# Optimization experiments

Measured on AMD Instinct MI355X. Metric: run time of the kernel, lower is better.

## Reference

```python
import jax, jax.numpy as jnp
import numpy as np

EPS = 1e-5

def _layernorm(x, g, b):
    mu = jnp.mean(x, axis=-1, keepdims=True)
    var = jnp.mean(jnp.square(x - mu), axis=-1, keepdims=True)
    return (x - mu) * jax.lax.rsqrt(var + EPS) * g + b

def _time_shift(x):
    # xx[:, t] = x[:, t-1], xx[:, 0] = 0  (ZeroPad2d((0,0,1,-1)))
    return jnp.pad(x, ((0, 0), (1, 0), (0, 0)))[:, :-1, :]

def _wkv(time_decay, time_first, k, v):
    # Numerically-stable RWKV v4 recurrence (matches wkv_cuda forward).
    # k, v: [B, T, C]; time_decay, time_first: [C]
    w = -jnp.exp(time_decay)  # negative decay
    u = time_first
    B, T, C = k.shape
    aa0 = jnp.zeros((B, C), k.dtype)
    bb0 = jnp.zeros((B, C), k.dtype)
    pp0 = jnp.full((B, C), -1e38, k.dtype)

    def step(carry, kv_t):
        aa, bb, pp = carry
        kt, vt = kv_t
        ww = u + kt
        p = jnp.maximum(pp, ww)
        e1 = jnp.exp(pp - p)
        e2 = jnp.exp(ww - p)
        yt = (e1 * aa + e2 * vt) / (e1 * bb + e2)
        ww2 = pp + w
        p2 = jnp.maximum(ww2, kt)
        e1b = jnp.exp(ww2 - p2)
        e2b = jnp.exp(kt - p2)
        return (e1b * aa + e2b * vt, e1b * bb + e2b, p2), yt

    kT = jnp.swapaxes(k, 0, 1)  # [T, B, C]
    vT = jnp.swapaxes(v, 0, 1)
    _, y = jax.lax.scan(step, (aa0, bb0, pp0), (kT, vT))
    return jnp.swapaxes(y, 0, 1)  # [B, T, C]


def setup_inputs() -> dict:
    num_layers, layer_id, C = 8, 1, 512
    B, T = 512, 50
    H = 4 * C
    key = jax.random.key(0)
    ks = jax.random.split(key, 12)

    # parameter init mirroring the torch module's structured init
    ratio_0_to_1 = layer_id / (num_layers - 1)
    ratio_1_to_almost0 = 1.0 - layer_id / num_layers
    h = np.arange(C, dtype=np.float32)
    time_decay = (-5 + 8 * (h / (C - 1)) ** (0.7 + 1.3 * ratio_0_to_1)).astype(np.float32)
    zigzag = (np.array([(i + 1) % 3 - 1 for i in range(C)], dtype=np.float32)) * 0.5
    time_first = (np.ones(C, dtype=np.float32) * np.log(0.3) + zigzag).astype(np.float32)
    xr = (h / C).astype(np.float32)
    att_mix_k = (xr ** ratio_1_to_almost0)[None, None, :].astype(np.float32)
    att_mix_v = (xr ** ratio_1_to_almost0 + 0.3 * ratio_0_to_1)[None, None, :].astype(np.float32)
    att_mix_r = (xr ** (0.5 * ratio_1_to_almost0))[None, None, :].astype(np.float32)
    ffn_mix_k = att_mix_k.copy()
    ffn_mix_r = att_mix_k.copy()

    s = 0.02
    return {
        "x": jax.random.normal(ks[0], (B, T, C), jnp.float32),
        "ln1_g": jnp.ones((C,), jnp.float32), "ln1_b": jnp.zeros((C,), jnp.float32),
        "ln2_g": jnp.ones((C,), jnp.float32), "ln2_b": jnp.zeros((C,), jnp.float32),
        "att_mix_k": jnp.asarray(att_mix_k), "att_mix_v": jnp.asarray(att_mix_v),
        "att_mix_r": jnp.asarray(att_mix_r),
        "time_decay": jnp.asarray(time_decay), "time_first": jnp.asarray(time_first),
        "Wk": jax.random.normal(ks[1], (C, C), jnp.float32) * s,
        "Wv": jax.random.normal(ks[2], (C, C), jnp.float32) * s,
        "Wr": jax.random.normal(ks[3], (C, C), jnp.float32) * s,
        "Wo": jax.random.normal(ks[4], (C, C), jnp.float32) * s,
        "ffn_mix_k": jnp.asarray(ffn_mix_k), "ffn_mix_r": jnp.asarray(ffn_mix_r),
        "Fk": jax.random.normal(ks[5], (H, C), jnp.float32) * s,
        "Fv": jax.random.normal(ks[6], (C, H), jnp.float32) * s,
        "Fr": jax.random.normal(ks[7], (C, C), jnp.float32) * s,
    }


def reference(x, ln1_g, ln1_b, ln2_g, ln2_b,
              att_mix_k, att_mix_v, att_mix_r, time_decay, time_first,
              Wk, Wv, Wr, Wo, ffn_mix_k, ffn_mix_r, Fk, Fv, Fr):
    # --- time-mix (attention) branch ---
    h = _layernorm(x, ln1_g, ln1_b)
    hh = _time_shift(h)
    xk = h * att_mix_k + hh * (1 - att_mix_k)
    xv = h * att_mix_v + hh * (1 - att_mix_v)
    xr = h * att_mix_r + hh * (1 - att_mix_r)
    k = jnp.einsum('btc,dc->btd', xk, Wk)
    v = jnp.einsum('btc,dc->btd', xv, Wv)
    sr = jax.nn.sigmoid(jnp.einsum('btc,dc->btd', xr, Wr))
    rwkv = sr * _wkv(time_decay, time_first, k, v)
    x = x + jnp.einsum('btc,dc->btd', rwkv, Wo)

    # --- channel-mix (FFN) branch ---
    h = _layernorm(x, ln2_g, ln2_b)
    hh = _time_shift(h)
    fk = h * ffn_mix_k + hh * (1 - ffn_mix_k)
    fr = h * ffn_mix_r + hh * (1 - ffn_mix_r)
    kk = jnp.einsum('btc,hc->bth', fk, Fk)
    kk = jnp.square(jax.nn.relu(kk))
    kv = jnp.einsum('bth,ch->btc', kk, Fv)
    rkv = jax.nn.sigmoid(jnp.einsum('btc,dc->btd', fr, Fr)) * kv
    return x + rkv
```

## Files before the change

kernel.cpp:

```cpp
#include <hip/hip_runtime.h>
#include <stdint.h>

typedef unsigned short u16;
typedef __bf16 bf16x8 __attribute__((ext_vector_type(8)));
typedef float f32x4 __attribute__((ext_vector_type(4)));

#define DEV static __device__ __forceinline__

DEV u16 f2b(float f) {
    unsigned u = __float_as_uint(f);
    u += 0x7FFF + ((u >> 16) & 1);
    return (u16)(u >> 16);
}
DEV float b2f(u16 h) { return __uint_as_float((unsigned)h << 16); }

DEV void load16(const void* g, void* l) {
    __builtin_amdgcn_global_load_lds((const __attribute__((address_space(1))) void*)g,
                                     (__attribute__((address_space(3))) void*)l, 16, 0, 0);
}

__global__ __launch_bounds__(256) void cvt_all(
    const float* __restrict__ Wk, const float* __restrict__ Wv,
    const float* __restrict__ Wr, const float* __restrict__ Wo,
    const float* __restrict__ Fk, const float* __restrict__ Fv,
    const float* __restrict__ Fr, u16* __restrict__ dst) {
    const int CC = 512 * 512, HC = 2048 * 512;
    int e = (blockIdx.x * 256 + threadIdx.x) * 4;
    const float* s; int base;
    if      (e < 1 * CC)      { s = Wk; base = 0; }
    else if (e < 2 * CC)      { s = Wv; base = 1 * CC; }
    else if (e < 3 * CC)      { s = Wr; base = 2 * CC; }
    else if (e < 4 * CC)      { s = Wo; base = 3 * CC; }
    else if (e < 4 * CC + HC) { s = Fk; base = 4 * CC; }
    else if (e < 4 * CC + 2 * HC) { s = Fv; base = 4 * CC + HC; }
    else                      { s = Fr; base = 4 * CC + 2 * HC; }
    float4 f = *(const float4*)(s + (e - base));
    ushort4 o;
    o.x = f2b(f.x); o.y = f2b(f.y); o.z = f2b(f.z); o.w = f2b(f.w);
    *(ushort4*)(dst + e) = o;
}

template <int NOUT>
__global__ __launch_bounds__(256) void ln_seq(
    const float* __restrict__ x, const float* __restrict__ g, const float* __restrict__ be,
    const float* __restrict__ mk, const float* __restrict__ mv, const float* __restrict__ mr,
    u16* __restrict__ ok, u16* __restrict__ ov, u16* __restrict__ orr, int T) {
    const int C = 512;
    int b = blockIdx.x;
    int tid = threadIdx.x;
    int c = tid * 2;
    const float* xb = x + (size_t)b * T * C;
    float g0 = g[c], g1 = g[c + 1], be0 = be[c], be1 = be[c + 1];
    float k0 = mk[c], k1 = mk[c + 1];
    float v0 = 0.f, v1 = 0.f;
    if (NOUT == 3) { v0 = mv[c]; v1 = mv[c + 1]; }
    float r0 = mr[c], r1 = mr[c + 1];
    __shared__ float sm[2][8];
    float h0p = 0.f, h1p = 0.f;
    size_t idx = (size_t)b * T * C + c;
    for (int t = 0; t < T; ++t) {
        float2 vt = *(const float2*)(xb + (size_t)t * C + c);
        float s0 = vt.x + vt.y, s1 = vt.x * vt.x + vt.y * vt.y;
#pragma unroll
        for (int off = 32; off; off >>= 1) {
            s0 += __shfl_down(s0, off); s1 += __shfl_down(s1, off);
        }
        int w = tid >> 6;
        if ((tid & 63) == 0) { sm[t & 1][w * 2] = s0; sm[t & 1][w * 2 + 1] = s1; }
        __syncthreads();
        s0 = sm[t & 1][0] + sm[t & 1][2] + sm[t & 1][4] + sm[t & 1][6];
        s1 = sm[t & 1][1] + sm[t & 1][3] + sm[t & 1][5] + sm[t & 1][7];
        float mu = s0 * (1.f / 512.f);
        float var = s1 * (1.f / 512.f) - mu * mu;
        float rs = rsqrtf(var + 1e-5f);
        float h0 = (vt.x - mu) * rs * g0 + be0;
        float h1 = (vt.y - mu) * rs * g1 + be1;
        *(ushort2*)&ok[idx] = make_ushort2(f2b(h0 * k0 + h0p * (1.f - k0)),
                                           f2b(h1 * k1 + h1p * (1.f - k1)));
        if (NOUT == 3)
            *(ushort2*)&ov[idx] = make_ushort2(f2b(h0 * v0 + h0p * (1.f - v0)),
                                               f2b(h1 * v1 + h1p * (1.f - v1)));
        *(ushort2*)&orr[idx] = make_ushort2(f2b(h0 * r0 + h0p * (1.f - r0)),
                                            f2b(h1 * r1 + h1p * (1.f - r1)));
        h0p = h0; h1p = h1;
        idx += C;
    }
}

template <int EPI>
__global__ __launch_bounds__(256) void gemm128(
    const u16* __restrict__ A0, int strideAz,
    const u16* __restrict__ B0, int strideBz,
    void* O0, void* O1, void* O2,
    const float* __restrict__ Add, const u16* __restrict__ Mul,
    int K, int D) {
    const int BM = 128, BN = 128, BK = 64;
    __shared__ __align__(16) u16 As[2][BM * BK];
    __shared__ __align__(16) u16 Bs[2][BN * BK];

    int gx = gridDim.x, gy = gridDim.y;
    int fid = blockIdx.x + gx * (blockIdx.y + gy * blockIdx.z);
    int nwg = gx * gy * gridDim.z;
    int q = nwg >> 3, r = nwg & 7, xcd = fid & 7, jj = fid >> 3;
    int swz = (xcd < r ? xcd * (q + 1) : r * (q + 1) + (xcd - r) * q) + jj;
    int bx = swz % gx;
    int tmp = swz / gx;
    int by = tmp % gy;
    int bz = tmp / gy;

    const u16* A = A0 + (size_t)bz * strideAz;
    const u16* B = B0 + (size_t)bz * strideBz;
    void* Out = (bz == 0) ? O0 : (bz == 1) ? O1 : O2;

    int tid = threadIdx.x, lane = tid & 63, w = tid >> 6;
    int wm = w >> 1, wn = w & 1;
    int rowBase = by * BM, colBase = bx * BN;
    int l8 = lane >> 3;
    int gsrc = ((lane & 7) ^ l8) * 8;

    const int nt = K / BK;
    f32x4 acc[4][4] = {};

    auto stage = [&](int buf, int kt) {
#pragma unroll
        for (int i = 0; i < 4; ++i) {
            int rr0 = w * 32 + i * 8;
            load16(A + (size_t)(rowBase + rr0 + l8) * K + kt + gsrc, &As[buf][rr0 * BK]);
            load16(B + (size_t)(colBase + rr0 + l8) * K + kt + gsrc, &Bs[buf][rr0 * BK]);
        }
    };

    stage(0, 0);
    __syncthreads();
    int cur = 0;
    for (int t = 0; t < nt; ++t) {
        if (t + 1 < nt) stage(cur ^ 1, (t + 1) * BK);
#pragma unroll
        for (int s = 0; s < 2; ++s) {
            bf16x8 af[4], bfv[4];
#pragma unroll
            for (int m = 0; m < 4; ++m) {
                int row = wm * 64 + m * 16 + (lane & 15);
                int gsw = (s * 4 + (lane >> 4)) ^ (row & 7);
                af[m] = *(const bf16x8*)&As[cur][row * BK + gsw * 8];
            }
#pragma unroll
            for (int n = 0; n < 4; ++n) {
                int col = wn * 64 + n * 16 + (lane & 15);
                int gsw = (s * 4 + (lane >> 4)) ^ (col & 7);
                bfv[n] = *(const bf16x8*)&Bs[cur][col * BK + gsw * 8];
            }
#pragma unroll
            for (int m = 0; m < 4; ++m)
#pragma unroll
                for (int n = 0; n < 4; ++n)
                    acc[m][n] = __builtin_amdgcn_mfma_f32_16x16x32_bf16(af[m], bfv[n], acc[m][n], 0, 0, 0);
        }
        __syncthreads();
        cur ^= 1;
    }

    int r0e = (lane >> 4) * 4;
    int ce = lane & 15;
#pragma unroll
    for (int m = 0; m < 4; ++m) {
#pragma unroll
        for (int n = 0; n < 4; ++n) {
            int row = rowBase + wm * 64 + m * 16 + r0e;
            int col = colBase + wn * 64 + n * 16 + ce;
#pragma unroll
            for (int rr = 0; rr < 4; ++rr) {
                size_t idx = (size_t)(row + rr) * D + col;
                float v = acc[m][n][rr];
                if (EPI == 0) {
                    ((u16*)Out)[idx] = f2b(v);
                } else if (EPI == 2) {
                    ((float*)Out)[idx] = v + Add[idx];
                } else if (EPI == 3) {
                    float rl = fmaxf(v, 0.f);
                    ((u16*)Out)[idx] = f2b(rl * rl);
                } else if (EPI == 4) {
                    float s = 1.f / (1.f + __expf(-v));
                    ((float*)Out)[idx] = Add[idx] + s * b2f(Mul[idx]);
                } else {
                    ((u16*)Out)[idx] = (bz == 2) ? f2b(1.f / (1.f + __expf(-v))) : f2b(v);
                }
            }
        }
    }
}

__global__ __launch_bounds__(256) void wkv_kernel(
    const u16* __restrict__ k, const u16* __restrict__ v, const u16* __restrict__ sr,
    const float* __restrict__ td, const float* __restrict__ tf,
    u16* __restrict__ rwkv, int T) {
    const int C = 512;
    int gid = blockIdx.x * 256 + threadIdx.x;
    int c = gid & (C - 1);
    int b = gid >> 9;
    float w = -__expf(td[c]);
    float u = tf[c];
    float aa = 0.f, bb = 0.f, pp = -1e38f;
    size_t idx = (size_t)b * T * C + c;
    for (int t = 0; t < T; ++t, idx += C) {
        float kt = b2f(k[idx]), vt = b2f(v[idx]);
        float ww = u + kt;
        float p = fmaxf(pp, ww);
        float e1 = __expf(pp - p), e2 = __expf(ww - p);
        float y = (e1 * aa + e2 * vt) / (e1 * bb + e2);
        float ww2 = pp + w;
        float p2 = fmaxf(ww2, kt);
        float e1b = __expf(ww2 - p2), e2b = __expf(kt - p2);
        aa = e1b * aa + e2b * vt;
        bb = e1b * bb + e2b;
        pp = p2;
        rwkv[idx] = f2b(b2f(sr[idx]) * y);
    }
}

extern "C" void kernel_launch(void* const* d_in, const int* in_sizes, int n_in,
                              void* d_out, int out_size, void* d_ws, size_t ws_size,
                              hipStream_t stream) {
    const int B = 512, T = 50, C = 512, H = 2048;
    const int NT = B * T;

    const float* x     = (const float*)d_in[0];
    const float* ln1_g = (const float*)d_in[1];
    const float* ln1_b = (const float*)d_in[2];
    const float* ln2_g = (const float*)d_in[3];
    const float* ln2_b = (const float*)d_in[4];
    const float* amk   = (const float*)d_in[5];
    const float* amv   = (const float*)d_in[6];
    const float* amr   = (const float*)d_in[7];
    const float* td    = (const float*)d_in[8];
    const float* tf    = (const float*)d_in[9];
    const float* Wk    = (const float*)d_in[10];
    const float* Wv    = (const float*)d_in[11];
    const float* Wr    = (const float*)d_in[12];
    const float* Wo    = (const float*)d_in[13];
    const float* fmk   = (const float*)d_in[14];
    const float* fmr   = (const float*)d_in[15];
    const float* Fk    = (const float*)d_in[16];
    const float* Fv    = (const float*)d_in[17];
    const float* Fr    = (const float*)d_in[18];
    float* out = (float*)d_out;

    const size_t WBYTES = ((size_t)C*C*2)*6 + ((size_t)H*C*2)*2 + 4096;
    int R = 6400;
    if (ws_size >= (size_t)25600 * 1024 * 7 + WBYTES)      R = 25600;
    else if (ws_size >= (size_t)12800 * 1024 * 7 + WBYTES) R = 12800;
    const int NCH = NT / R;

    char* ws = (char*)d_ws;
    size_t off = 0;
    auto alloc = [&](size_t bytes) {
        char* p = ws + off;
        off += (bytes + 255) & ~(size_t)255;
        return p;
    };
    const size_t uc = (size_t)R * C * 2;
    u16*   U0 = (u16*)alloc(uc);
    u16*   U1 = (u16*)alloc(uc);
    u16*   U2 = (u16*)alloc(uc);
    u16*   U3 = (u16*)alloc(uc);
    u16*   U4 = (u16*)alloc(uc);
    float* X2 = (float*)alloc((size_t)R * C * 4);
    u16*   U5 = (u16*)X2;
    u16* bWkvr = (u16*)alloc((size_t)3 * C * C * 2);
    u16* bWo   = (u16*)alloc((size_t)C * C * 2);
    u16* bFk   = (u16*)alloc((size_t)H * C * 2);
    u16* bFv   = (u16*)alloc((size_t)C * H * 2);
    u16* bFr   = (u16*)alloc((size_t)C * C * 2);
    u16* kk = U0;

    cvt_all<<<(5 * C * C + 2 * H * C) / 1024, 256, 0, stream>>>(
        Wk, Wv, Wr, Wo, Fk, Fv, Fr, bWkvr);

    for (int ch = 0; ch < NCH; ++ch) {
        const float* xc  = x   + (size_t)ch * R * C;
        float*       oc  = out + (size_t)ch * R * C;

        ln_seq<3><<<R / T, 256, 0, stream>>>(xc, ln1_g, ln1_b, amk, amv, amr, U0, U1, U2, T);
        gemm128<5><<<dim3(C / 128, R / 128, 3), 256, 0, stream>>>(
            U0, R * C, bWkvr, C * C, U3, U4, U5, nullptr, nullptr, C, C);
        wkv_kernel<<<(R / T) * C / 256, 256, 0, stream>>>(U3, U4, U5, td, tf, U0, T);
        gemm128<2><<<dim3(C / 128, R / 128, 1), 256, 0, stream>>>(
            U0, 0, bWo, 0, X2, nullptr, nullptr, xc, nullptr, C, C);

        ln_seq<2><<<R / T, 256, 0, stream>>>(X2, ln2_g, ln2_b, fmk, nullptr, fmr, U3, nullptr, U4, T);
        for (int hh = 0; hh < 2; ++hh) {
            size_t ro = (size_t)hh * (R / 2);
            gemm128<3><<<dim3(H / 128, R / 256, 1), 256, 0, stream>>>(
                U3 + ro * C, 0, bFk, 0, kk, nullptr, nullptr, nullptr, nullptr, C, H);
            gemm128<0><<<dim3(C / 128, R / 256, 1), 256, 0, stream>>>(
                kk, 0, bFv, 0, U2 + ro * C, nullptr, nullptr, nullptr, nullptr, H, C);
        }
        gemm128<4><<<dim3(C / 128, R / 128, 1), 256, 0, stream>>>(
            U4, 0, bFr, 0, oc, nullptr, nullptr, X2, U2, C, C);
    }
}
```

Baseline: 579.6 us.

## Split layernorm over time chunks and single-buffer GEMM LDS tiles

The layernorm plus time-shift kernel now launches five blocks per sequence, each covering ten timesteps and recomputing one preceding row to supply the shifted value, which multiplies parallelism by five. Separately, the GEMM drops its double-buffered LDS staging for a single buffer with a sync after each load. That halves LDS use and may allow more resident blocks per CU, but it removes the overlap between global loads and MFMA compute.

```diff
diff --git a/kernel.cpp b/kernel.cpp
--- a/kernel.cpp
+++ b/kernel.cpp
@@ -41,12 +41,14 @@
 }
 
 template <int NOUT>
-__global__ __launch_bounds__(256) void ln_seq(
+__global__ __launch_bounds__(256) void ln_chunk(
     const float* __restrict__ x, const float* __restrict__ g, const float* __restrict__ be,
     const float* __restrict__ mk, const float* __restrict__ mv, const float* __restrict__ mr,
     u16* __restrict__ ok, u16* __restrict__ ov, u16* __restrict__ orr, int T) {
-    const int C = 512;
-    int b = blockIdx.x;
+    const int C = 512, TC = 10;
+    int nch = T / TC;
+    int b = blockIdx.x / nch;
+    int t0 = (blockIdx.x % nch) * TC;
     int tid = threadIdx.x;
     int c = tid * 2;
     const float* xb = x + (size_t)b * T * C;
@@ -57,8 +59,8 @@
     float r0 = mr[c], r1 = mr[c + 1];
     __shared__ float sm[2][8];
     float h0p = 0.f, h1p = 0.f;
-    size_t idx = (size_t)b * T * C + c;
-    for (int t = 0; t < T; ++t) {
+    int tstart = (t0 == 0) ? 0 : t0 - 1;
+    for (int t = tstart; t < t0 + TC; ++t) {
         float2 vt = *(const float2*)(xb + (size_t)t * C + c);
         float s0 = vt.x + vt.y, s1 = vt.x * vt.x + vt.y * vt.y;
 #pragma unroll
@@ -75,15 +77,17 @@
         float rs = rsqrtf(var + 1e-5f);
         float h0 = (vt.x - mu) * rs * g0 + be0;
         float h1 = (vt.y - mu) * rs * g1 + be1;
-        *(ushort2*)&ok[idx] = make_ushort2(f2b(h0 * k0 + h0p * (1.f - k0)),
-                                           f2b(h1 * k1 + h1p * (1.f - k1)));
-        if (NOUT == 3)
-            *(ushort2*)&ov[idx] = make_ushort2(f2b(h0 * v0 + h0p * (1.f - v0)),
-                                               f2b(h1 * v1 + h1p * (1.f - v1)));
-        *(ushort2*)&orr[idx] = make_ushort2(f2b(h0 * r0 + h0p * (1.f - r0)),
-                                            f2b(h1 * r1 + h1p * (1.f - r1)));
+        if (t >= t0) {
+            size_t idx = (size_t)b * T * C + (size_t)t * C + c;
+            *(ushort2*)&ok[idx] = make_ushort2(f2b(h0 * k0 + h0p * (1.f - k0)),
+                                               f2b(h1 * k1 + h1p * (1.f - k1)));
+            if (NOUT == 3)
+                *(ushort2*)&ov[idx] = make_ushort2(f2b(h0 * v0 + h0p * (1.f - v0)),
+                                                   f2b(h1 * v1 + h1p * (1.f - v1)));
+            *(ushort2*)&orr[idx] = make_ushort2(f2b(h0 * r0 + h0p * (1.f - r0)),
+                                                f2b(h1 * r1 + h1p * (1.f - r1)));
+        }
         h0p = h0; h1p = h1;
-        idx += C;
     }
 }
 
@@ -95,8 +99,8 @@
     const float* __restrict__ Add, const u16* __restrict__ Mul,
     int K, int D) {
     const int BM = 128, BN = 128, BK = 64;
-    __shared__ __align__(16) u16 As[2][BM * BK];
-    __shared__ __align__(16) u16 Bs[2][BN * BK];
+    __shared__ __align__(16) u16 As[BM * BK];
+    __shared__ __align__(16) u16 Bs[BN * BK];
 
     int gx = gridDim.x, gy = gridDim.y;
     int fid = blockIdx.x + gx * (blockIdx.y + gy * blockIdx.z);
@@ -121,20 +125,15 @@
     const int nt = K / BK;
     f32x4 acc[4][4] = {};
 
-    auto stage = [&](int buf, int kt) {
+    for (int t = 0; t < nt; ++t) {
+        int kt = t * BK;
 #pragma unroll
         for (int i = 0; i < 4; ++i) {
             int rr0 = w * 32 + i * 8;
-            load16(A + (size_t)(rowBase + rr0 + l8) * K + kt + gsrc, &As[buf][rr0 * BK]);
-            load16(B + (size_t)(colBase + rr0 + l8) * K + kt + gsrc, &Bs[buf][rr0 * BK]);
-        }
-    };
-
-    stage(0, 0);
-    __syncthreads();
-    int cur = 0;
-    for (int t = 0; t < nt; ++t) {
-        if (t + 1 < nt) stage(cur ^ 1, (t + 1) * BK);
+            load16(A + (size_t)(rowBase + rr0 + l8) * K + kt + gsrc, &As[rr0 * BK]);
+            load16(B + (size_t)(colBase + rr0 + l8) * K + kt + gsrc, &Bs[rr0 * BK]);
+        }
+        __syncthreads();
 #pragma unroll
         for (int s = 0; s < 2; ++s) {
             bf16x8 af[4], bfv[4];
@@ -142,13 +141,13 @@
             for (int m = 0; m < 4; ++m) {
                 int row = wm * 64 + m * 16 + (lane & 15);
                 int gsw = (s * 4 + (lane >> 4)) ^ (row & 7);
-                af[m] = *(const bf16x8*)&As[cur][row * BK + gsw * 8];
+                af[m] = *(const bf16x8*)&As[row * BK + gsw * 8];
             }
 #pragma unroll
             for (int n = 0; n < 4; ++n) {
                 int col = wn * 64 + n * 16 + (lane & 15);
                 int gsw = (s * 4 + (lane >> 4)) ^ (col & 7);
-                bfv[n] = *(const bf16x8*)&Bs[cur][col * BK + gsw * 8];
+                bfv[n] = *(const bf16x8*)&Bs[col * BK + gsw * 8];
             }
 #pragma unroll
             for (int m = 0; m < 4; ++m)
@@ -157,7 +156,6 @@
                     acc[m][n] = __builtin_amdgcn_mfma_f32_16x16x32_bf16(af[m], bfv[n], acc[m][n], 0, 0, 0);
         }
         __syncthreads();
-        cur ^= 1;
     }
 
     int r0e = (lane >> 4) * 4;
@@ -280,14 +278,14 @@
         const float* xc  = x   + (size_t)ch * R * C;
         float*       oc  = out + (size_t)ch * R * C;
 
-        ln_seq<3><<<R / T, 256, 0, stream>>>(xc, ln1_g, ln1_b, amk, amv, amr, U0, U1, U2, T);
+        ln_chunk<3><<<(R / T) * 5, 256, 0, stream>>>(xc, ln1_g, ln1_b, amk, amv, amr, U0, U1, U2, T);
         gemm128<5><<<dim3(C / 128, R / 128, 3), 256, 0, stream>>>(
             U0, R * C, bWkvr, C * C, U3, U4, U5, nullptr, nullptr, C, C);
         wkv_kernel<<<(R / T) * C / 256, 256, 0, stream>>>(U3, U4, U5, td, tf, U0, T);
         gemm128<2><<<dim3(C / 128, R / 128, 1), 256, 0, stream>>>(
             U0, 0, bWo, 0, X2, nullptr, nullptr, xc, nullptr, C, C);
 
-        ln_seq<2><<<R / T, 256, 0, stream>>>(X2, ln2_g, ln2_b, fmk, nullptr, fmr, U3, nullptr, U4, T);
+        ln_chunk<2><<<(R / T) * 5, 256, 0, stream>>>(X2, ln2_g, ln2_b, fmk, nullptr, fmr, U3, nullptr, U4, T);
         for (int hh = 0; hh < 2; ++hh) {
             size_t ro = (size_t)hh * (R / 2);
             gemm128<3><<<dim3(H / 128, R / 256, 1), 256, 0, stream>>>(
```

Result: no change. 571.9 us (-1.3%).
